# Kernel optimization log

Hardware: AMD Instinct MI355X
Metric: run time of the kernel (lower is better)

The kernel has to match this reference:

```python
import jax, jax.numpy as jnp
import numpy as np

D_MODEL = 1024
D_INNER = 4096
K = 127
B, L = 2, 4096

def setup_inputs() -> dict:
    key = jax.random.key(0)
    k1, k2, k3, k4, k5 = jax.random.split(key, 5)
    x = jax.random.normal(k1, (B, L, D_MODEL), dtype=jnp.float32)
    # in_proj: Linear(d, 2*m) -> weight [2m, d] (torch convention)
    w_in = jax.random.normal(k2, (2 * D_INNER, D_MODEL), dtype=jnp.float32) * (1.0 / np.sqrt(D_MODEL))
    # depthwise conv weight: [m, 1, k] in torch; store as [m, k]
    w_dw = jax.random.normal(k3, (D_INNER, K), dtype=jnp.float32) * (1.0 / np.sqrt(K))
    b_dw = jax.random.normal(k4, (D_INNER,), dtype=jnp.float32) * 0.01
    # out_proj: Linear(m, d) -> weight [d, m]
    w_out = jax.random.normal(k5, (D_MODEL, D_INNER), dtype=jnp.float32) * (1.0 / np.sqrt(D_INNER))
    return {"x": x, "w_in": w_in, "w_dw": w_dw, "b_dw": b_dw, "w_out": w_out}

def _causal_dwconv(v, w_dw, b_dw):
    # v: [B, L, m]; causal depthwise conv with kernel K
    # pad K-1 on the left only (equivalent to torch pad=K-1 then [..., :L])
    v_bcl = jnp.transpose(v, (0, 2, 1))  # [B, m, L]
    out = jax.lax.conv_general_dilated(
        v_bcl,
        w_dw[:, None, :],  # [m, 1, K]
        window_strides=(1,),
        padding=[(K - 1, 0)],
        feature_group_count=D_INNER,
        dimension_numbers=("NCH", "OIH", "NCH"),
    )
    out = out + b_dw[None, :, None]
    return jnp.transpose(out, (0, 2, 1))  # [B, L, m]

def reference(x, w_in, w_dw, b_dw, w_out):
    vg = jnp.einsum("bld,ed->ble", x, w_in)  # [B, L, 2m]
    v, g = jnp.split(vg, 2, axis=-1)
    v = _causal_dwconv(v, w_dw, b_dw)
    y = jax.nn.silu(v) * jax.nn.silu(g)
    return jnp.einsum("blm,dm->bld", y, w_out)
```

## Files before the change

### kernel.cpp

```cpp
#include <hip/hip_runtime.h>
#include <hip/hip_bf16.h>
#include <cstdint>
#include <cstddef>

typedef __fp16 f16_t;
typedef __attribute__((ext_vector_type(8))) __fp16 f16x8;
typedef __attribute__((ext_vector_type(4))) __fp16 f16x4;
typedef __attribute__((ext_vector_type(2))) __fp16 h2_t;
typedef __attribute__((ext_vector_type(4))) float floatx4;

__device__ __forceinline__ void async_copy_16B(const void* g, void* l) {
  __builtin_amdgcn_global_load_lds(
      (const __attribute__((address_space(1))) void*)g,
      (__attribute__((address_space(3))) void*)l, 16, 0, 0);
}

__global__ __launch_bounds__(256) void prep(
    const float* __restrict__ x, const float* __restrict__ w_in,
    const float* __restrict__ w_out, const float* __restrict__ w_dw,
    f16_t* __restrict__ x_h, f16_t* __restrict__ wi_h,
    f16_t* __restrict__ wo_h, h2_t* __restrict__ wp) {
  const int tid = blockIdx.x * 256 + threadIdx.x;
  if (tid < 5242880) {
    const float* src;
    f16_t* dst;
    int off;
    if (tid < 2097152) {
      src = x; dst = x_h; off = tid;
    } else if (tid < 4194304) {
      src = w_in; dst = wi_h; off = tid - 2097152;
    } else {
      src = w_out; dst = wo_h; off = tid - 4194304;
    }
    const float4 v = *(const float4*)(src + (size_t)off * 4);
    f16x4 o;
    o.x = (f16_t)v.x; o.y = (f16_t)v.y; o.z = (f16_t)v.z; o.w = (f16_t)v.w;
    *(f16x4*)(dst + (size_t)off * 4) = o;
  } else {
    const int idx = tid - 5242880;
    if (idx < 128 * 4096) {
      const int p = idx >> 12;
      const int c = idx & 4095;
      float a, b;
      if (p < 126) {
        a = w_dw[c * 127 + p]; b = w_dw[c * 127 + p + 1];
      } else if (p == 126) {
        a = w_dw[c * 127 + 126]; b = 0.f;
      } else {
        a = 0.f; b = w_dw[c * 127 + 0];
      }
      h2_t w;
      w.x = (f16_t)a; w.y = (f16_t)b;
      wp[idx] = w;
    }
  }
}

__global__ __launch_bounds__(512, 2) void gemm256_8p(
    const f16_t* __restrict__ A, const f16_t* __restrict__ B,
    f16_t* __restrict__ C, int M, int N, int K) {
  extern __shared__ char smem[];
  const int t = threadIdx.x;
  const int lane = t & 63;
  const int wave = t >> 6;
  const int wm = wave >> 2;
  const int wn = wave & 3;

  const int bid = blockIdx.x;
  const int xcd = bid & 7;
  const int l = bid >> 3;
  const int quad = l >> 5;
  const int qm = (l >> 3) & 3;
  const int qn = l & 7;
  const int m0 = ((xcd >> 1) * 8 + (quad >> 1) * 4 + qm) * 256;
  const int n0 = ((xcd & 1) * 16 + (quad & 1) * 8 + qn) * 256;

  const int fr = lane & 15;
  const int ks = lane >> 4;

  auto stageB = [&](int d, int k0, int half) {
#pragma unroll
    for (int u = 0; u < 2; ++u) {
      const int q = u * 512 + t;
      const int row = half * 128 + (q >> 3);
      const int slot = q & 7;
      const int col = (slot ^ (row & 7)) * 8;
      async_copy_16B(B + (size_t)(n0 + row) * K + k0 + col,
                     smem + d * 65536 + 32768 + row * 128 + slot * 16);
    }
  };
  auto stageA = [&](int d, int k0, int j) {
    const int blk = t >> 8;
    const int row = j * 32 + blk * 128 + ((t & 255) >> 3);
    const int slot = t & 7;
    const int col = (slot ^ (row & 7)) * 8;
    async_copy_16B(A + (size_t)(m0 + row) * K + k0 + col,
                   smem + d * 65536 + row * 128 + slot * 16);
  };
  auto ldA = [&](int d, int R, int kslot) -> f16x8 {
    return *(const f16x8*)(smem + d * 65536 + R * 128 +
                           ((kslot ^ (R & 7)) << 4));
  };
  auto ldB = [&](int d, int R, int kslot) -> f16x8 {
    return *(const f16x8*)(smem + d * 65536 + 32768 + R * 128 +
                           ((kslot ^ (R & 7)) << 4));
  };

  floatx4 acc[8][4] = {};
  const int kTiles = K / 64;

  stageB(0, 0, 0); stageB(0, 0, 1);
  stageA(0, 0, 0); stageA(0, 0, 1); stageA(0, 0, 2); stageA(0, 0, 3);
  stageB(1, 64, 0); stageA(1, 64, 0);
  stageB(1, 64, 1); stageA(1, 64, 1);
  stageA(1, 64, 2);
  asm volatile("s_waitcnt vmcnt(7)" ::: "memory");
  __builtin_amdgcn_s_barrier();

  f16x8 bf[4][2];
  for (int tt = 0; tt < kTiles; ++tt) {
    const int d = tt & 1;
    const int k1 = (tt + 1) * 64;
    const int k2 = (tt + 2) * 64;
    const bool pf1 = (tt + 1 < kTiles);
    const bool pf2 = (tt + 2 < kTiles);
#pragma unroll
    for (int q = 0; q < 4; ++q) {
      f16x8 af[2][2];
#pragma unroll
      for (int kh = 0; kh < 2; ++kh) {
#pragma unroll
        for (int ii = 0; ii < 2; ++ii)
          af[ii][kh] = ldA(d, wm * 128 + q * 32 + ii * 16 + fr, kh * 4 + ks);
        if (q == 0)
#pragma unroll
          for (int j = 0; j < 4; ++j)
            bf[j][kh] = ldB(d, wn * 64 + j * 16 + fr, kh * 4 + ks);
      }
      if (q == 0) {
        if (pf1) stageA(d ^ 1, k1, 3);
      } else if (q == 1) {
        if (pf2) { stageB(d, k2, 0); stageA(d, k2, 0); }
      } else if (q == 2) {
        if (pf2) { stageB(d, k2, 1); stageA(d, k2, 1); }
      } else {
        if (pf2) {
          stageA(d, k2, 2);
          asm volatile("s_waitcnt vmcnt(7)" ::: "memory");
        } else if (pf1) {
          asm volatile("s_waitcnt vmcnt(0)" ::: "memory");
        }
      }
      __builtin_amdgcn_s_barrier();
      asm volatile("s_waitcnt lgkmcnt(0)" ::: "memory");
      __builtin_amdgcn_s_setprio(1);
#pragma unroll
      for (int kh = 0; kh < 2; ++kh)
#pragma unroll
        for (int ii = 0; ii < 2; ++ii)
#pragma unroll
          for (int j = 0; j < 4; ++j)
            acc[q * 2 + ii][j] = __builtin_amdgcn_mfma_f32_16x16x32_f16(
                af[ii][kh], bf[j][kh], acc[q * 2 + ii][j], 0, 0, 0);
      __builtin_amdgcn_s_setprio(0);
      __builtin_amdgcn_s_barrier();
    }
  }

  const int cr = (lane >> 4) * 4;
  const int cc = lane & 15;
#pragma unroll
  for (int i = 0; i < 8; ++i)
#pragma unroll
    for (int j = 0; j < 4; ++j)
#pragma unroll
      for (int r = 0; r < 4; ++r) {
        const int row = m0 + wm * 128 + i * 16 + cr + r;
        const int col = n0 + wn * 64 + j * 16 + cc;
        C[(size_t)row * N + col] = (f16_t)acc[i][j][r];
      }
}

__global__ __launch_bounds__(256) void gemm_bt_k128(
    const f16_t* __restrict__ A, const f16_t* __restrict__ B,
    float* __restrict__ C, int M, int N, int K) {
  constexpr int BM_ = 128, BN_ = 64, KP = 4;
  constexpr int NA = BM_ * 4 * KP;
  constexpr int NTOT = (BM_ + BN_) * 4 * KP;
  constexpr int CPT = NTOT / 256;

  __shared__ f16_t smem[(BM_ + BN_) * 128];
  const int t = threadIdx.x;
  const int lane = t & 63;
  const int wave = t >> 6;
  const int m0 = blockIdx.y * BM_;
  const int n0 = blockIdx.x * BN_;
  const int wr = wave * 32;
  const int fr = lane & 15;
  const int fk = (lane >> 4) * 8;

  floatx4 acc[2][4] = {};

  const int kTiles = K / 128;
  for (int kt = 0; kt < kTiles; ++kt) {
    const int k0 = kt * 128;
    __syncthreads();
#pragma unroll
    for (int it = 0; it < CPT; ++it) {
      const int p = it * 256 + t;
      const f16_t* gsrc;
      if (p < NA) {
        const int h = p >> 9;
        const int r = (p >> 2) & (BM_ - 1);
        const int kc = h * 32 + (p & 3) * 8;
        gsrc = A + (size_t)(m0 + r) * K + k0 + kc;
      } else {
        const int q = p - NA;
        const int h = q >> 8;
        const int r = (q >> 2) & (BN_ - 1);
        const int kc = h * 32 + (q & 3) * 8;
        gsrc = B + (size_t)(n0 + r) * K + k0 + kc;
      }
      async_copy_16B(gsrc, smem + p * 8);
    }
    __syncthreads();

#pragma unroll
    for (int h = 0; h < KP; ++h) {
      f16x8 af[2], bf[4];
#pragma unroll
      for (int i = 0; i < 2; ++i)
        af[i] = *(const f16x8*)(smem + h * BM_ * 32 + (wr + i * 16 + fr) * 32 + fk);
#pragma unroll
      for (int j = 0; j < 4; ++j)
        bf[j] = *(const f16x8*)(smem + NA * 8 + h * BN_ * 32 + (j * 16 + fr) * 32 + fk);
#pragma unroll
      for (int i = 0; i < 2; ++i)
#pragma unroll
        for (int j = 0; j < 4; ++j)
          acc[i][j] = __builtin_amdgcn_mfma_f32_16x16x32_f16(
              af[i], bf[j], acc[i][j], 0, 0, 0);
    }
  }

  const int cr = (lane >> 4) * 4;
  const int cc = lane & 15;
#pragma unroll
  for (int i = 0; i < 2; ++i)
#pragma unroll
    for (int j = 0; j < 4; ++j)
#pragma unroll
      for (int r = 0; r < 4; ++r) {
        const int row = m0 + wr + i * 16 + cr + r;
        const int col = n0 + j * 16 + cc;
        C[(size_t)row * N + col] = acc[i][j][r];
      }
}

#define CONV_L 128
#define CPAIRS 127

__global__ __launch_bounds__(256) void conv_gate(
    const f16_t* __restrict__ vg, const h2_t* __restrict__ wp,
    const float* __restrict__ b_dw, f16_t* __restrict__ y) {
  __shared__ uint32_t vtp[CPAIRS * 64];
  __shared__ uint32_t wpl[128 * 64];
  const int t = threadIdx.x;
  const int lane = t & 63;
  const int wave = t >> 6;
  const int c0 = blockIdx.x * 64;
  const int lt = blockIdx.y & 31;
  const int b = blockIdx.y >> 5;
  const int l0 = lt * CONV_L;

#pragma unroll
  for (int it = 0; it < 8; ++it) {
    const int q = it * 256 + t;
    async_copy_16B(wp + (size_t)(q >> 4) * 4096 + c0 + (q & 15) * 4,
                   wpl + q * 4);
  }
  for (int q = t; q < CPAIRS * 8; q += 256) {
    const int m = q >> 3;
    const int oc = (q & 7) * 8;
    const int le = l0 - 126 + 2 * m;
    uint4 a = make_uint4(0u, 0u, 0u, 0u);
    uint4 bb = make_uint4(0u, 0u, 0u, 0u);
    if (le >= 0) {
      const size_t base = (size_t)(b * 4096 + le) * 8192 + c0 + oc;
      a = *(const uint4*)(vg + base);
      bb = *(const uint4*)(vg + base + 8192);
    }
    uint32_t* dst = vtp + m * 64 + oc;
    const uint32_t aw[4] = {a.x, a.y, a.z, a.w};
    const uint32_t bw[4] = {bb.x, bb.y, bb.z, bb.w};
#pragma unroll
    for (int i = 0; i < 4; ++i) {
      dst[2 * i] = (aw[i] & 0xFFFFu) | (bw[i] << 16);
      dst[2 * i + 1] = (aw[i] >> 16) | (bw[i] & 0xFFFF0000u);
    }
  }

  const int c = c0 + lane;
  const int lb = l0 + wave * 32;
  const f16_t* gp = vg + (size_t)(b * 4096 + lb) * 8192 + 4096 + c;
  f16_t gvals[32];
#pragma unroll
  for (int i = 0; i < 32; ++i) gvals[i] = gp[(size_t)i * 8192];

  __syncthreads();

  const float bias = b_dw[c];
  float acc[32];
#pragma unroll
  for (int i = 0; i < 32; ++i) acc[i] = bias;

  const uint32_t* vbase = vtp + wave * 16 * 64 + lane;
  const uint32_t* wbase = wpl + lane;

  h2_t ring[17];
#pragma unroll
  for (int m = 0; m < 17; ++m)
    ring[m] = __builtin_bit_cast(h2_t, vbase[m * 64]);

  {
    const h2_t w0 = __builtin_bit_cast(h2_t, wbase[127 * 64]);
#pragma unroll
    for (int h = 0; h < 16; ++h)
      acc[2 * h + 1] =
          __builtin_amdgcn_fdot2(w0, ring[h], acc[2 * h + 1], false);
  }

#pragma unroll
  for (int k = 0; k < 64; ++k) {
    const h2_t we = __builtin_bit_cast(h2_t, wbase[(2 * k) * 64]);
#pragma unroll
    for (int h = 0; h < 16; ++h)
      acc[2 * h] =
          __builtin_amdgcn_fdot2(we, ring[(k + h) % 17], acc[2 * h], false);
    if (k < 63) {
      const h2_t wo = __builtin_bit_cast(h2_t, wbase[(2 * k + 1) * 64]);
#pragma unroll
      for (int h = 0; h < 16; ++h)
        acc[2 * h + 1] = __builtin_amdgcn_fdot2(wo, ring[(k + 1 + h) % 17],
                                                acc[2 * h + 1], false);
      if (k < 62)
        ring[k % 17] = __builtin_bit_cast(h2_t, vbase[(17 + k) * 64]);
    }
  }

  f16_t* yp = y + (size_t)(b * 4096 + lb) * 4096 + c;
#pragma unroll
  for (int i = 0; i < 32; ++i) {
    const float gv = (float)gvals[i];
    const float v = acc[i];
    const float sv = v / (1.f + __expf(-v));
    const float sg = gv / (1.f + __expf(-gv));
    yp[(size_t)i * 4096] = (f16_t)(sv * sg);
  }
}

extern "C" void kernel_launch(void* const* d_in, const int* in_sizes, int n_in,
                              void* d_out, int out_size, void* d_ws,
                              size_t ws_size, hipStream_t stream) {
  const float* x     = (const float*)d_in[0];
  const float* w_in  = (const float*)d_in[1];
  const float* w_dw  = (const float*)d_in[2];
  const float* b_dw  = (const float*)d_in[3];
  const float* w_out = (const float*)d_in[4];
  float* out = (float*)d_out;

  char* p = (char*)d_ws;
  f16_t* x_h  = (f16_t*)p; p += (size_t)8192 * 1024 * 2;
  f16_t* wi_h = (f16_t*)p; p += (size_t)8192 * 1024 * 2;
  f16_t* wo_h = (f16_t*)p; p += (size_t)1024 * 4096 * 2;
  h2_t*  wp   = (h2_t*)p;  p += (size_t)128 * 4096 * 4;
  f16_t* vg   = (f16_t*)p; p += (size_t)8192 * 8192 * 2;
  f16_t* y    = (f16_t*)p; p += (size_t)8192 * 4096 * 2;

  prep<<<22528, 256, 0, stream>>>(x, w_in, w_out, w_dw, x_h, wi_h, wo_h, wp);

  hipFuncSetAttribute(reinterpret_cast<const void*>(gemm256_8p),
                      hipFuncAttributeMaxDynamicSharedMemorySize, 131072);
  gemm256_8p<<<1024, 512, 131072, stream>>>(x_h, wi_h, vg, 8192, 8192, 1024);

  conv_gate<<<dim3(64, 64), 256, 0, stream>>>(vg, wp, b_dw, y);
  gemm_bt_k128<<<dim3(16, 64), 256, 0, stream>>>(y, wo_h, out,
                                                 8192, 1024, 4096);
}
```

Measured before the change: 495.0 us.

## Simplify in-proj GEMM pipeline and retile out-proj GEMM to 256x128 double-buffered

The in-projection GEMM drops its 8-phase interleaved prefetch schedule. In its place is a plain double buffer: the next full tile is loaded each iteration, then one barrier and a full MFMA sweep follow. The out-projection GEMM moves from a small 128x64 single-buffered tile to a 256x128 tile with 512 threads, XCD-aware block mapping, swizzled LDS and async double buffering. This raises data reuse and overlaps loads with math. The in-proj change may lose some of the finer load/compute overlap the phased schedule gave, and the out-proj grid shrinks to 256 blocks.

```diff
diff --git a/kernel.cpp b/kernel.cpp
--- a/kernel.cpp
+++ b/kernel.cpp
@@ -56,7 +56,7 @@
   }
 }
 
-__global__ __launch_bounds__(512, 2) void gemm256_8p(
+__global__ __launch_bounds__(512, 2) void gemm256_1p(
     const f16_t* __restrict__ A, const f16_t* __restrict__ B,
     f16_t* __restrict__ C, int M, int N, int K) {
   extern __shared__ char smem[];
@@ -78,25 +78,24 @@
   const int fr = lane & 15;
   const int ks = lane >> 4;
 
-  auto stageB = [&](int d, int k0, int half) {
-#pragma unroll
-    for (int u = 0; u < 2; ++u) {
+  auto stageTile = [&](int d, int k0) {
+#pragma unroll
+    for (int u = 0; u < 4; ++u) {
       const int q = u * 512 + t;
-      const int row = half * 128 + (q >> 3);
-      const int slot = q & 7;
+      const int row = q >> 3, slot = q & 7;
+      const int col = (slot ^ (row & 7)) * 8;
+      async_copy_16B(A + (size_t)(m0 + row) * K + k0 + col,
+                     smem + d * 65536 + row * 128 + slot * 16);
+    }
+#pragma unroll
+    for (int u = 0; u < 4; ++u) {
+      const int q = u * 512 + t;
+      const int row = q >> 3, slot = q & 7;
       const int col = (slot ^ (row & 7)) * 8;
       async_copy_16B(B + (size_t)(n0 + row) * K + k0 + col,
                      smem + d * 65536 + 32768 + row * 128 + slot * 16);
     }
   };
-  auto stageA = [&](int d, int k0, int j) {
-    const int blk = t >> 8;
-    const int row = j * 32 + blk * 128 + ((t & 255) >> 3);
-    const int slot = t & 7;
-    const int col = (slot ^ (row & 7)) * 8;
-    async_copy_16B(A + (size_t)(m0 + row) * K + k0 + col,
-                   smem + d * 65536 + row * 128 + slot * 16);
-  };
   auto ldA = [&](int d, int R, int kslot) -> f16x8 {
     return *(const f16x8*)(smem + d * 65536 + R * 128 +
                            ((kslot ^ (R & 7)) << 4));
@@ -109,62 +108,40 @@
   floatx4 acc[8][4] = {};
   const int kTiles = K / 64;
 
-  stageB(0, 0, 0); stageB(0, 0, 1);
-  stageA(0, 0, 0); stageA(0, 0, 1); stageA(0, 0, 2); stageA(0, 0, 3);
-  stageB(1, 64, 0); stageA(1, 64, 0);
-  stageB(1, 64, 1); stageA(1, 64, 1);
-  stageA(1, 64, 2);
-  asm volatile("s_waitcnt vmcnt(7)" ::: "memory");
-  __builtin_amdgcn_s_barrier();
-
-  f16x8 bf[4][2];
+  stageTile(0, 0);
   for (int tt = 0; tt < kTiles; ++tt) {
     const int d = tt & 1;
-    const int k1 = (tt + 1) * 64;
-    const int k2 = (tt + 2) * 64;
-    const bool pf1 = (tt + 1 < kTiles);
-    const bool pf2 = (tt + 2 < kTiles);
-#pragma unroll
-    for (int q = 0; q < 4; ++q) {
-      f16x8 af[2][2];
-#pragma unroll
-      for (int kh = 0; kh < 2; ++kh) {
-#pragma unroll
-        for (int ii = 0; ii < 2; ++ii)
-          af[ii][kh] = ldA(d, wm * 128 + q * 32 + ii * 16 + fr, kh * 4 + ks);
-        if (q == 0)
-#pragma unroll
-          for (int j = 0; j < 4; ++j)
-            bf[j][kh] = ldB(d, wn * 64 + j * 16 + fr, kh * 4 + ks);
-      }
-      if (q == 0) {
-        if (pf1) stageA(d ^ 1, k1, 3);
-      } else if (q == 1) {
-        if (pf2) { stageB(d, k2, 0); stageA(d, k2, 0); }
-      } else if (q == 2) {
-        if (pf2) { stageB(d, k2, 1); stageA(d, k2, 1); }
-      } else {
-        if (pf2) {
-          stageA(d, k2, 2);
-          asm volatile("s_waitcnt vmcnt(7)" ::: "memory");
-        } else if (pf1) {
-          asm volatile("s_waitcnt vmcnt(0)" ::: "memory");
-        }
-      }
-      __builtin_amdgcn_s_barrier();
-      asm volatile("s_waitcnt lgkmcnt(0)" ::: "memory");
-      __builtin_amdgcn_s_setprio(1);
+    const bool pf = (tt + 1 < kTiles);
+    if (pf) {
+      stageTile(d ^ 1, (tt + 1) * 64);
+      asm volatile("s_waitcnt vmcnt(8)" ::: "memory");
+    } else {
+      asm volatile("s_waitcnt vmcnt(0)" ::: "memory");
+    }
+    __builtin_amdgcn_s_barrier();
+
+    f16x8 bf[4][2];
+#pragma unroll
+    for (int j = 0; j < 4; ++j)
 #pragma unroll
       for (int kh = 0; kh < 2; ++kh)
-#pragma unroll
-        for (int ii = 0; ii < 2; ++ii)
-#pragma unroll
-          for (int j = 0; j < 4; ++j)
-            acc[q * 2 + ii][j] = __builtin_amdgcn_mfma_f32_16x16x32_f16(
-                af[ii][kh], bf[j][kh], acc[q * 2 + ii][j], 0, 0, 0);
-      __builtin_amdgcn_s_setprio(0);
-      __builtin_amdgcn_s_barrier();
-    }
+        bf[j][kh] = ldB(d, wn * 64 + j * 16 + fr, kh * 4 + ks);
+    __builtin_amdgcn_s_setprio(1);
+#pragma unroll
+    for (int ii = 0; ii < 8; ++ii) {
+      const f16x8 af0 = ldA(d, wm * 128 + ii * 16 + fr, ks);
+      const f16x8 af1 = ldA(d, wm * 128 + ii * 16 + fr, 4 + ks);
+#pragma unroll
+      for (int j = 0; j < 4; ++j)
+        acc[ii][j] = __builtin_amdgcn_mfma_f32_16x16x32_f16(
+            af0, bf[j][0], acc[ii][j], 0, 0, 0);
+#pragma unroll
+      for (int j = 0; j < 4; ++j)
+        acc[ii][j] = __builtin_amdgcn_mfma_f32_16x16x32_f16(
+            af1, bf[j][1], acc[ii][j], 0, 0, 0);
+    }
+    __builtin_amdgcn_s_setprio(0);
+    __builtin_amdgcn_s_barrier();
   }
 
   const int cr = (lane >> 4) * 4;
@@ -181,78 +158,101 @@
       }
 }
 
-__global__ __launch_bounds__(256) void gemm_bt_k128(
+__global__ __launch_bounds__(512, 2) void gemmN128_1p(
     const f16_t* __restrict__ A, const f16_t* __restrict__ B,
     float* __restrict__ C, int M, int N, int K) {
-  constexpr int BM_ = 128, BN_ = 64, KP = 4;
-  constexpr int NA = BM_ * 4 * KP;
-  constexpr int NTOT = (BM_ + BN_) * 4 * KP;
-  constexpr int CPT = NTOT / 256;
-
-  __shared__ f16_t smem[(BM_ + BN_) * 128];
+  extern __shared__ char smem[];
   const int t = threadIdx.x;
   const int lane = t & 63;
   const int wave = t >> 6;
-  const int m0 = blockIdx.y * BM_;
-  const int n0 = blockIdx.x * BN_;
-  const int wr = wave * 32;
+  const int wm = wave >> 2;
+  const int wn = wave & 3;
+
+  const int bid = blockIdx.x;
+  const int xcd = bid & 7;
+  const int l = bid >> 3;
+  const int m0 = (xcd * 4 + (l >> 3)) * 256;
+  const int n0 = (l & 7) * 128;
+
   const int fr = lane & 15;
-  const int fk = (lane >> 4) * 8;
-
-  floatx4 acc[2][4] = {};
-
-  const int kTiles = K / 128;
-  for (int kt = 0; kt < kTiles; ++kt) {
-    const int k0 = kt * 128;
-    __syncthreads();
-#pragma unroll
-    for (int it = 0; it < CPT; ++it) {
-      const int p = it * 256 + t;
-      const f16_t* gsrc;
-      if (p < NA) {
-        const int h = p >> 9;
-        const int r = (p >> 2) & (BM_ - 1);
-        const int kc = h * 32 + (p & 3) * 8;
-        gsrc = A + (size_t)(m0 + r) * K + k0 + kc;
-      } else {
-        const int q = p - NA;
-        const int h = q >> 8;
-        const int r = (q >> 2) & (BN_ - 1);
-        const int kc = h * 32 + (q & 3) * 8;
-        gsrc = B + (size_t)(n0 + r) * K + k0 + kc;
-      }
-      async_copy_16B(gsrc, smem + p * 8);
-    }
-    __syncthreads();
-
-#pragma unroll
-    for (int h = 0; h < KP; ++h) {
-      f16x8 af[2], bf[4];
-#pragma unroll
-      for (int i = 0; i < 2; ++i)
-        af[i] = *(const f16x8*)(smem + h * BM_ * 32 + (wr + i * 16 + fr) * 32 + fk);
-#pragma unroll
-      for (int j = 0; j < 4; ++j)
-        bf[j] = *(const f16x8*)(smem + NA * 8 + h * BN_ * 32 + (j * 16 + fr) * 32 + fk);
-#pragma unroll
-      for (int i = 0; i < 2; ++i)
-#pragma unroll
-        for (int j = 0; j < 4; ++j)
-          acc[i][j] = __builtin_amdgcn_mfma_f32_16x16x32_f16(
-              af[i], bf[j], acc[i][j], 0, 0, 0);
-    }
+  const int ks = lane >> 4;
+
+  auto stageTile = [&](int d, int k0) {
+#pragma unroll
+    for (int u = 0; u < 4; ++u) {
+      const int q = u * 512 + t;
+      const int row = q >> 3, slot = q & 7;
+      const int col = (slot ^ (row & 7)) * 8;
+      async_copy_16B(A + (size_t)(m0 + row) * K + k0 + col,
+                     smem + d * 49152 + row * 128 + slot * 16);
+    }
+#pragma unroll
+    for (int u = 0; u < 2; ++u) {
+      const int q = u * 512 + t;
+      const int row = q >> 3, slot = q & 7;
+      const int col = (slot ^ (row & 7)) * 8;
+      async_copy_16B(B + (size_t)(n0 + row) * K + k0 + col,
+                     smem + d * 49152 + 32768 + row * 128 + slot * 16);
+    }
+  };
+  auto ldA = [&](int d, int R, int kslot) -> f16x8 {
+    return *(const f16x8*)(smem + d * 49152 + R * 128 +
+                           ((kslot ^ (R & 7)) << 4));
+  };
+  auto ldB = [&](int d, int R, int kslot) -> f16x8 {
+    return *(const f16x8*)(smem + d * 49152 + 32768 + R * 128 +
+                           ((kslot ^ (R & 7)) << 4));
+  };
+
+  floatx4 acc[8][2] = {};
+  const int kTiles = K / 64;
+
+  stageTile(0, 0);
+  for (int tt = 0; tt < kTiles; ++tt) {
+    const int d = tt & 1;
+    const bool pf = (tt + 1 < kTiles);
+    if (pf) {
+      stageTile(d ^ 1, (tt + 1) * 64);
+      asm volatile("s_waitcnt vmcnt(6)" ::: "memory");
+    } else {
+      asm volatile("s_waitcnt vmcnt(0)" ::: "memory");
+    }
+    __builtin_amdgcn_s_barrier();
+
+    f16x8 bf[2][2];
+#pragma unroll
+    for (int j = 0; j < 2; ++j)
+#pragma unroll
+      for (int kh = 0; kh < 2; ++kh)
+        bf[j][kh] = ldB(d, wn * 32 + j * 16 + fr, kh * 4 + ks);
+    __builtin_amdgcn_s_setprio(1);
+#pragma unroll
+    for (int ii = 0; ii < 8; ++ii) {
+      const f16x8 af0 = ldA(d, wm * 128 + ii * 16 + fr, ks);
+      const f16x8 af1 = ldA(d, wm * 128 + ii * 16 + fr, 4 + ks);
+#pragma unroll
+      for (int j = 0; j < 2; ++j)
+        acc[ii][j] = __builtin_amdgcn_mfma_f32_16x16x32_f16(
+            af0, bf[j][0], acc[ii][j], 0, 0, 0);
+#pragma unroll
+      for (int j = 0; j < 2; ++j)
+        acc[ii][j] = __builtin_amdgcn_mfma_f32_16x16x32_f16(
+            af1, bf[j][1], acc[ii][j], 0, 0, 0);
+    }
+    __builtin_amdgcn_s_setprio(0);
+    __builtin_amdgcn_s_barrier();
   }
 
   const int cr = (lane >> 4) * 4;
   const int cc = lane & 15;
 #pragma unroll
-  for (int i = 0; i < 2; ++i)
-#pragma unroll
-    for (int j = 0; j < 4; ++j)
+  for (int i = 0; i < 8; ++i)
+#pragma unroll
+    for (int j = 0; j < 2; ++j)
 #pragma unroll
       for (int r = 0; r < 4; ++r) {
-        const int row = m0 + wr + i * 16 + cr + r;
-        const int col = n0 + j * 16 + cc;
+        const int row = m0 + wm * 128 + i * 16 + cr + r;
+        const int col = n0 + wn * 32 + j * 16 + cc;
         C[(size_t)row * N + col] = acc[i][j][r];
       }
 }
@@ -379,11 +379,13 @@
 
   prep<<<22528, 256, 0, stream>>>(x, w_in, w_out, w_dw, x_h, wi_h, wo_h, wp);
 
-  hipFuncSetAttribute(reinterpret_cast<const void*>(gemm256_8p),
+  hipFuncSetAttribute(reinterpret_cast<const void*>(gemm256_1p),
                       hipFuncAttributeMaxDynamicSharedMemorySize, 131072);
-  gemm256_8p<<<1024, 512, 131072, stream>>>(x_h, wi_h, vg, 8192, 8192, 1024);
+  gemm256_1p<<<1024, 512, 131072, stream>>>(x_h, wi_h, vg, 8192, 8192, 1024);
 
   conv_gate<<<dim3(64, 64), 256, 0, stream>>>(vg, wp, b_dw, y);
-  gemm_bt_k128<<<dim3(16, 64), 256, 0, stream>>>(y, wo_h, out,
-                                                 8192, 1024, 4096);
-}
+
+  hipFuncSetAttribute(reinterpret_cast<const void*>(gemmN128_1p),
+                      hipFuncAttributeMaxDynamicSharedMemorySize, 98304);
+  gemmN128_1p<<<256, 512, 98304, stream>>>(y, wo_h, out, 8192, 1024, 4096);
+}
```

Measured after the change: 444.4 us. -10.2%, faster.
